# Kernel tuning notes

Hardware: AMD Instinct MI355X
Metric: run time of the kernel (lower is better)

Reference implementation:

```python
import jax, jax.numpy as jnp
import numpy as np

HEADS = 16
HIDDEN = 1024
DH = HIDDEN // HEADS
STD = 0.02


def setup_inputs() -> dict:
    key = jax.random.key(0)
    ks = jax.random.split(key, 12)
    B, S = 4, 2048
    inp = {
        'q': jax.random.normal(ks[0], (B, S, HIDDEN), jnp.float32),
        'k': jax.random.normal(ks[1], (B, S, HIDDEN), jnp.float32),
        'v': jax.random.normal(ks[2], (B, S, HIDDEN), jnp.float32),
        'mask': jax.random.randint(ks[3], (B, S), 0, 2, jnp.int32),
        # linear layers: weight [out,in] torch-style, init N(0, 0.02), bias 0
        'wq': STD * jax.random.normal(ks[4], (HIDDEN, HIDDEN), jnp.float32),
        'bq': jnp.zeros((HIDDEN,), jnp.float32),
        'wk': STD * jax.random.normal(ks[5], (HIDDEN, HIDDEN), jnp.float32),
        'bk': jnp.zeros((HIDDEN,), jnp.float32),
        'wv': STD * jax.random.normal(ks[6], (HIDDEN, HIDDEN), jnp.float32),
        'bv': jnp.zeros((HIDDEN,), jnp.float32),
        'wo': STD * jax.random.normal(ks[7], (HIDDEN, HIDDEN), jnp.float32),
        'bo': jnp.zeros((HIDDEN,), jnp.float32),
    }
    return inp


def _split_heads(x):
    B, S, _ = x.shape
    return x.reshape(B, S, HEADS, DH).transpose(0, 2, 1, 3)  # [B,H,S,dh]


def reference(q, k, v, mask, wq, bq, wk, bk, wv, bv, wo, bo):
    B, S, _ = q.shape
    qh = _split_heads(q @ wq.T + bq)
    kh = _split_heads(k @ wk.T + bk)
    vh = _split_heads(v @ wv.T + bv)
    scale = 1.0 / jnp.sqrt(jnp.float32(DH))
    corr = jnp.einsum('bhqd,bhkd->bhqk', qh, kh) * scale  # [B,H,S,S]
    # original masks QUERY rows: mask [B,S] -> [B,1,S,1] broadcast over heads & keys
    row_mask = (mask != 0)[:, None, :, None]
    corr = jnp.where(row_mask, corr, jnp.float32(-1e9))
    prob = jax.nn.softmax(corr, axis=-1)
    # dropout p=0.0 (eval / deterministic reference)
    hidden = jnp.einsum('bhqk,bhkd->bhqd', prob, vh)
    hidden = hidden.transpose(0, 2, 1, 3).reshape(B, S, HIDDEN)
    return hidden @ wo.T + bo
```

## Files before the change

kernel.cpp:

```cpp
#include <hip/hip_runtime.h>

#define BATCH 4
#define SEQ 2048
#define HEADS 16
#define DHEAD 64
#define HID 1024
#define MROWS (BATCH * SEQ)
#define QSCALE 0.1803368801111092f

typedef unsigned short u16;
typedef unsigned int u32;
typedef __attribute__((ext_vector_type(4))) float f32x4;
typedef __attribute__((ext_vector_type(8))) short bf16x8;

#define MFMA16(a, b, c) __builtin_amdgcn_mfma_f32_16x16x32_bf16((a), (b), (c), 0, 0, 0)
#define EXP2F(x) __builtin_amdgcn_exp2f(x)

__device__ __forceinline__ u16 f2bf(float f) {
  union { float f; u32 i; } x; x.f = f;
  u32 r = x.i + 0x7fffu + ((x.i >> 16) & 1u);
  return (u16)(r >> 16);
}

__device__ __forceinline__ void lds16(const u16* g, u16* s) {
  __builtin_amdgcn_global_load_lds(
      (const __attribute__((address_space(1))) void*)g,
      (__attribute__((address_space(3))) void*)s, 16, 0, 0);
}

__device__ __forceinline__ void stage8f(const float* __restrict__ g, u16* s) {
  const float4 a = *(const float4*)g;
  const float4 b = *(const float4*)(g + 4);
  ushort4 lo, hi;
  lo.x = f2bf(a.x); lo.y = f2bf(a.y); lo.z = f2bf(a.z); lo.w = f2bf(a.w);
  hi.x = f2bf(b.x); hi.y = f2bf(b.y); hi.z = f2bf(b.z); hi.w = f2bf(b.w);
  *(ushort4*)s = lo;
  *(ushort4*)(s + 4) = hi;
}

struct CvtArgs {
  const float* src[7];
  u16* dst[7];
};
__global__ __launch_bounds__(256) void cvt7(CvtArgs args, int yoff, int nact) {
  const int y = blockIdx.y + yoff;
  const int i = (blockIdx.x * 256 + threadIdx.x) * 8;
  if (y < 3) {
    if (i < nact) stage8f(args.src[y] + i, args.dst[y] + i);
  } else {
    if (i < 4 * (1 << 20)) {
      const int j = i >> 20, off = i & ((1 << 20) - 1);
      stage8f(args.src[3 + j] + off, args.dst[3 + j] + off);
    }
  }
}

template<bool ADMA, bool BDMA>
__device__ __forceinline__ void gemm_core(
    const void* __restrict__ Av, const void* __restrict__ Wv,
    int tid, int m0, int n0, u16* As, u16* Bs, f32x4 (&acc)[4][4])
{
  const int srow = tid >> 2, cslot = tid & 3;
  const int gc = cslot ^ ((srow >> 1) & 3);
  const int w = tid >> 6, l = tid & 63;
  const int quad = l >> 4, l15 = l & 15;
  const int sw = (l15 >> 1) & 3;
  const int wm = (w & 1) << 6, wn = (w >> 1) << 6;

  for (int k0 = 0; k0 < HID; k0 += 32) {
    if (ADMA) {
      const u16* ag = (const u16*)Av + (size_t)(m0 + srow) * HID + k0 + gc * 8;
      lds16(ag, &As[tid * 8]);
      lds16(ag + (size_t)64 * HID, &As[2048 + tid * 8]);
    } else {
      const float* ag = (const float*)Av + (size_t)(m0 + srow) * HID + k0 + gc * 8;
      stage8f(ag, &As[srow * 32 + cslot * 8]);
      stage8f(ag + (size_t)64 * HID, &As[(64 + srow) * 32 + cslot * 8]);
    }
    if (BDMA) {
      const u16* bg = (const u16*)Wv + (size_t)(n0 + srow) * HID + k0 + gc * 8;
      lds16(bg, &Bs[tid * 8]);
      lds16(bg + (size_t)64 * HID, &Bs[2048 + tid * 8]);
    } else {
      const float* bg = (const float*)Wv + (size_t)(n0 + srow) * HID + k0 + gc * 8;
      stage8f(bg, &Bs[srow * 32 + cslot * 8]);
      stage8f(bg + (size_t)64 * HID, &Bs[(64 + srow) * 32 + cslot * 8]);
    }
    __syncthreads();

    bf16x8 a[4], b[4];
    #pragma unroll
    for (int i = 0; i < 4; ++i)
      a[i] = *(const bf16x8*)&As[(wm + i * 16 + l15) * 32 + (quad ^ sw) * 8];
    #pragma unroll
    for (int j = 0; j < 4; ++j)
      b[j] = *(const bf16x8*)&Bs[(wn + j * 16 + l15) * 32 + (quad ^ sw) * 8];
    #pragma unroll
    for (int i = 0; i < 4; ++i)
      #pragma unroll
      for (int j = 0; j < 4; ++j)
        acc[i][j] = MFMA16(a[i], b[j], acc[i][j]);
    __syncthreads();
  }
}

template<bool ADMA, bool BDMA>
__global__ __launch_bounds__(256) void gemm_qkv(
    const void* __restrict__ xq, const void* __restrict__ xk,
    const void* __restrict__ xv,
    const void* __restrict__ wqv, const void* __restrict__ wkv,
    const void* __restrict__ wvv,
    const float* __restrict__ bq, const float* __restrict__ bk,
    const float* __restrict__ bv, const int* __restrict__ Mask,
    u16* __restrict__ qh, u16* __restrict__ kh, u16* __restrict__ vt)
{
  __shared__ u16 As[128 * 32];
  __shared__ u16 Bs[128 * 32];
  const int z = blockIdx.z;
  const void* A = (z == 0) ? xq : (z == 1) ? xk : xv;
  const void* W = (z == 0) ? wqv : (z == 1) ? wkv : wvv;
  const float* Bias = (z == 0) ? bq : (z == 1) ? bk : bv;

  const int tid = threadIdx.x;
  const int m0 = blockIdx.x << 7, n0 = blockIdx.y << 7;
  f32x4 acc[4][4] = {};
  gemm_core<ADMA, BDMA>(A, W, tid, m0, n0, As, Bs, acc);

  const int w = tid >> 6, l = tid & 63;
  const int quad = l >> 4, l15 = l & 15;
  const int wm = (w & 1) << 6, wn = (w >> 1) << 6;

  if (z <= 1) {
    u16* Out = (z == 0) ? qh : kh;
    #pragma unroll
    for (int i = 0; i < 4; ++i) {
      float fl[4];
      #pragma unroll
      for (int r = 0; r < 4; ++r) {
        const int m = m0 + wm + i * 16 + (quad << 2) + r;
        fl[r] = (z == 0) ? (Mask[m] ? QSCALE : 0.f) : 1.f;
      }
      #pragma unroll
      for (int j = 0; j < 4; ++j) {
        const int n = n0 + wn + j * 16 + l15;
        const float bias = Bias[n];
        const int h = n >> 6, d = n & 63;
        #pragma unroll
        for (int r = 0; r < 4; ++r) {
          const int m = m0 + wm + i * 16 + (quad << 2) + r;
          const int bb = m >> 11, s = m & (SEQ - 1);
          Out[((size_t)(bb * HEADS + h) * SEQ + s) * DHEAD + d] =
              f2bf((acc[i][j][r] + bias) * fl[r]);
        }
      }
    }
  } else {
    const int sblk = (m0 + wm) & (SEQ - 1);
    const int bb = (m0 + wm) >> 11;
    #pragma unroll
    for (int j = 0; j < 4; ++j) {
      const int n = n0 + wn + j * 16 + l15;
      const float bias = Bias[n];
      const int h = n >> 6, d = n & 63;
      u16* base = vt + ((size_t)(bb * HEADS + h) * DHEAD + d) * SEQ + sblk;
      #pragma unroll
      for (int r = 0; r < 4; ++r) {
        ushort4 pk;
        pk.x = f2bf(acc[0][j][r] + bias);
        pk.y = f2bf(acc[1][j][r] + bias);
        pk.z = f2bf(acc[2][j][r] + bias);
        pk.w = f2bf(acc[3][j][r] + bias);
        *(ushort4*)(base + ((quad << 2) + r) * 4) = pk;
      }
    }
  }
}

template<bool BDMA>
__global__ __launch_bounds__(256) void gemm_out(
    const u16* __restrict__ hidden, const void* __restrict__ wov,
    const float* __restrict__ bo, float* __restrict__ Out)
{
  __shared__ u16 As[128 * 32];
  __shared__ u16 Bs[128 * 32];
  const int tid = threadIdx.x;
  const int m0 = blockIdx.x << 7, n0 = blockIdx.y << 7;
  f32x4 acc[4][4] = {};
  gemm_core<true, BDMA>(hidden, wov, tid, m0, n0, As, Bs, acc);

  const int w = tid >> 6, l = tid & 63;
  const int quad = l >> 4, l15 = l & 15;
  const int wm = (w & 1) << 6, wn = (w >> 1) << 6;
  #pragma unroll
  for (int j = 0; j < 4; ++j) {
    const int n = n0 + wn + j * 16 + l15;
    const float bias = bo[n];
    #pragma unroll
    for (int i = 0; i < 4; ++i) {
      const int mb = m0 + wm + i * 16 + (quad << 2);
      #pragma unroll
      for (int r = 0; r < 4; ++r)
        Out[(size_t)(mb + r) * HID + n] = acc[i][j][r] + bias;
    }
  }
}

__global__ __launch_bounds__(128, 2) void attn_mfma(
    const u16* __restrict__ QH, const u16* __restrict__ KH,
    const u16* __restrict__ VT, u16* __restrict__ Hidden)
{
  __shared__ u16 QP[128 * 64];
  __shared__ u16 Ks[2][64 * 32];
  __shared__ u16 Vt[2][64 * 32];

  const int tid = threadIdx.x;
  const int w = tid >> 6, l = tid & 63;
  const int quad = l >> 4, l15 = l & 15;
  const int sw = (l15 >> 1) & 3;
  const int srow = tid >> 2, cslot = tid & 3;
  const int gc = cslot ^ ((srow >> 1) & 3);

  const int lin = blockIdx.y * 16 + blockIdx.x;
  const int bh = lin & 63, b = bh >> 4, h = bh & 15;
  const int q0 = (lin >> 6) << 7;

  const u16* qbase = QH + (size_t)bh * SEQ * DHEAD;
  const u16* kbase = KH + (size_t)bh * SEQ * DHEAD;
  const u16* vbase = VT + (size_t)bh * DHEAD * SEQ;

  #pragma unroll
  for (int hh = 0; hh < 2; ++hh)
    #pragma unroll
    for (int part = 0; part < 4; ++part)
      lds16(qbase + (size_t)(q0 + part * 32 + srow) * DHEAD + hh * 32 + gc * 8,
            &QP[hh * 4096 + part * 1024 + tid * 8]);
  __syncthreads();

  bf16x8 aq[2][4];
  #pragma unroll
  for (int hh = 0; hh < 2; ++hh)
    #pragma unroll
    for (int i = 0; i < 4; ++i)
      aq[hh][i] = *(const bf16x8*)
          &QP[hh * 4096 + (w * 64 + i * 16 + l15) * 32 + (quad ^ sw) * 8];

  float lsum[4][4] = {};
  f32x4 o[4][4] = {};

  for (int t0 = 0; t0 < SEQ; t0 += 64) {
    __syncthreads();
    #pragma unroll
    for (int hh = 0; hh < 2; ++hh)
      #pragma unroll
      for (int part = 0; part < 2; ++part) {
        lds16(kbase + (size_t)(t0 + part * 32 + srow) * DHEAD + hh * 32 + gc * 8,
              &Ks[hh][part * 1024 + tid * 8]);
        lds16(vbase + (size_t)(part * 32 + srow) * SEQ + t0 + hh * 32 + gc * 8,
              &Vt[hh][part * 1024 + tid * 8]);
      }
    __syncthreads();

    f32x4 s[4][4] = {};
    #pragma unroll
    for (int j = 0; j < 4; ++j)
      #pragma unroll
      for (int hh = 0; hh < 2; ++hh) {
        const bf16x8 bk = *(const bf16x8*)
            &Ks[hh][(j * 16 + l15) * 32 + (quad ^ sw) * 8];
        #pragma unroll
        for (int i = 0; i < 4; ++i)
          s[i][j] = MFMA16(aq[hh][i], bk, s[i][j]);
      }

    #pragma unroll
    for (int i = 0; i < 4; ++i)
      #pragma unroll
      for (int r = 0; r < 4; ++r) {
        const float p0 = EXP2F(s[i][0][r]);
        const float p1 = EXP2F(s[i][1][r]);
        const float p2 = EXP2F(s[i][2][r]);
        const float p3 = EXP2F(s[i][3][r]);
        lsum[i][r] += (p0 + p1) + (p2 + p3);
        const int row = w * 64 + i * 16 + (quad << 2) + r;
        const int cs = ((l15 >> 1) ^ (row & 7)) * 8 + (l15 & 1) * 4;
        ushort4 pk;
        pk.x = f2bf(p0); pk.y = f2bf(p1); pk.z = f2bf(p2); pk.w = f2bf(p3);
        *(ushort4*)&QP[row * 64 + cs] = pk;
      }

    #pragma unroll
    for (int hh = 0; hh < 2; ++hh) {
      bf16x8 ap[4];
      #pragma unroll
      for (int i = 0; i < 4; ++i) {
        const int row = w * 64 + i * 16 + l15;
        ap[i] = *(const bf16x8*)
            &QP[row * 64 + (((hh * 4 + quad) ^ (row & 7)) << 3)];
      }
      #pragma unroll
      for (int j = 0; j < 4; ++j) {
        const bf16x8 vb = *(const bf16x8*)
            &Vt[hh][(j * 16 + l15) * 32 + (quad ^ sw) * 8];
        #pragma unroll
        for (int i = 0; i < 4; ++i)
          o[i][j] = MFMA16(ap[i], vb, o[i][j]);
      }
    }
  }

  float inv[4][4];
  #pragma unroll
  for (int i = 0; i < 4; ++i)
    #pragma unroll
    for (int r = 0; r < 4; ++r) {
      float t = lsum[i][r];
      #pragma unroll
      for (int off = 1; off < 16; off <<= 1)
        t += __shfl_xor(t, off);
      inv[i][r] = 1.f / t;
    }

  #pragma unroll
  for (int i = 0; i < 4; ++i)
    #pragma unroll
    for (int j = 0; j < 4; ++j)
      #pragma unroll
      for (int r = 0; r < 4; ++r) {
        const int qrow = q0 + w * 64 + i * 16 + (quad << 2) + r;
        Hidden[((size_t)(b * SEQ + qrow)) * HID + h * DHEAD + j * 16 + l15] =
            f2bf(o[i][j][r] * inv[i][r]);
      }
}

extern "C" void kernel_launch(void* const* d_in, const int* in_sizes, int n_in,
                              void* d_out, int out_size, void* d_ws, size_t ws_size,
                              hipStream_t stream) {
  const float* q  = (const float*)d_in[0];
  const float* k  = (const float*)d_in[1];
  const float* v  = (const float*)d_in[2];
  const int* mask = (const int*)d_in[3];
  const float* wq = (const float*)d_in[4];
  const float* bq = (const float*)d_in[5];
  const float* wk = (const float*)d_in[6];
  const float* bk = (const float*)d_in[7];
  const float* wv = (const float*)d_in[8];
  const float* bv = (const float*)d_in[9];
  const float* wo = (const float*)d_in[10];
  const float* bo = (const float*)d_in[11];

  const size_t SEG = (size_t)MROWS * HID;
  const size_t WSEG = (size_t)HID * HID;
  const dim3 gq(MROWS / 128, HID / 128, 3);
  const dim3 go(MROWS / 128, HID / 128);
  const dim3 ga(SEQ / 128, BATCH * HEADS);

  const size_t planFULL = (6 * SEG + 4 * WSEG) * sizeof(u16);
  const size_t planMID  = (4 * SEG + 4 * WSEG) * sizeof(u16);

  if (ws_size >= planFULL) {
    u16* qb  = (u16*)d_ws;
    u16* kb  = qb + SEG;
    u16* vb  = kb + SEG;
    u16* qh  = vb + SEG;
    u16* kh  = qh + SEG;
    u16* vt  = kh + SEG;
    u16* wqb = vt + SEG;
    u16* wkb = wqb + WSEG;
    u16* wvb = wkb + WSEG;
    u16* wob = wvb + WSEG;
    u16* hidden = qb;

    CvtArgs ca;
    ca.src[0] = q;  ca.dst[0] = qb;
    ca.src[1] = k;  ca.dst[1] = kb;
    ca.src[2] = v;  ca.dst[2] = vb;
    ca.src[3] = wq; ca.dst[3] = wqb;
    ca.src[4] = wk; ca.dst[4] = wkb;
    ca.src[5] = wv; ca.dst[5] = wvb;
    ca.src[6] = wo; ca.dst[6] = wob;
    cvt7<<<dim3(SEG / 2048, 4), 256, 0, stream>>>(ca, 0, (int)SEG);

    gemm_qkv<true, true><<<gq, 256, 0, stream>>>(qb, kb, vb, wqb, wkb, wvb,
                                                 bq, bk, bv, mask, qh, kh, vt);
    attn_mfma<<<ga, 128, 0, stream>>>(qh, kh, vt, hidden);
    gemm_out<true><<<go, 256, 0, stream>>>(hidden, wob, bo, (float*)d_out);
  } else if (ws_size >= planMID) {
    u16* wqb = (u16*)d_ws;
    u16* wkb = wqb + WSEG;
    u16* wvb = wkb + WSEG;
    u16* wob = wvb + WSEG;
    u16* qh = wob + WSEG;
    u16* kh = qh + SEG;
    u16* vt = kh + SEG;
    u16* hidden = vt + SEG;

    CvtArgs ca;
    ca.src[0] = ca.src[1] = ca.src[2] = q;
    ca.dst[0] = ca.dst[1] = ca.dst[2] = wqb;
    ca.src[3] = wq; ca.dst[3] = wqb;
    ca.src[4] = wk; ca.dst[4] = wkb;
    ca.src[5] = wv; ca.dst[5] = wvb;
    ca.src[6] = wo; ca.dst[6] = wob;
    cvt7<<<dim3(4 * WSEG / 2048, 1), 256, 0, stream>>>(ca, 3, 0);

    gemm_qkv<false, true><<<gq, 256, 0, stream>>>(q, k, v, wqb, wkb, wvb,
                                                  bq, bk, bv, mask, qh, kh, vt);
    attn_mfma<<<ga, 128, 0, stream>>>(qh, kh, vt, hidden);
    gemm_out<true><<<go, 256, 0, stream>>>(hidden, wob, bo, (float*)d_out);
  } else {
    u16* qh = (u16*)d_ws;
    u16* kh = qh + SEG;
    u16* vt = kh + SEG;
    u16* hidden = vt + SEG;

    gemm_qkv<false, false><<<gq, 256, 0, stream>>>(q, k, v, wq, wk, wv,
                                                   bq, bk, bv, mask, qh, kh, vt);
    attn_mfma<<<ga, 128, 0, stream>>>(qh, kh, vt, hidden);
    gemm_out<false><<<go, 256, 0, stream>>>(hidden, wo, bo, (float*)d_out);
  }
}
```

Before: 358.0 us.

## Software-pipeline K/V loads in attention loop with double-buffered V and vmcnt waits

Restructures the attention main loop so the next K tile and the next V tile are issued with async global-to-LDS loads right after the QK^T MFMAs. V is double-buffered, and explicit s_waitcnt vmcnt counts with raw barriers replace the full __syncthreads pairs, so loads overlap the softmax and PV compute. It also adds s_setprio around the MFMA phases and replaces the manual bf16 rounding with the packed v_cvt_pk_bf16_f32 instruction in the V projection epilogue and the P store. This relies on careful vmcnt accounting: the last iteration issues a wraparound prefetch that is never used, which adds extra loads.

```diff
diff --git a/kernel.cpp b/kernel.cpp
--- a/kernel.cpp
+++ b/kernel.cpp
@@ -12,6 +12,7 @@
 typedef unsigned int u32;
 typedef __attribute__((ext_vector_type(4))) float f32x4;
 typedef __attribute__((ext_vector_type(8))) short bf16x8;
+typedef __attribute__((ext_vector_type(2))) unsigned int u32x2;
 
 #define MFMA16(a, b, c) __builtin_amdgcn_mfma_f32_16x16x32_bf16((a), (b), (c), 0, 0, 0)
 #define EXP2F(x) __builtin_amdgcn_exp2f(x)
@@ -20,6 +21,12 @@
   union { float f; u32 i; } x; x.f = f;
   u32 r = x.i + 0x7fffu + ((x.i >> 16) & 1u);
   return (u16)(r >> 16);
+}
+
+__device__ __forceinline__ u32 cvtpk(float a, float b) {
+  u32 d;
+  asm("v_cvt_pk_bf16_f32 %0, %1, %2" : "=v"(d) : "v"(a), "v"(b));
+  return d;
 }
 
 __device__ __forceinline__ void lds16(const u16* g, u16* s) {
@@ -165,12 +172,10 @@
       u16* base = vt + ((size_t)(bb * HEADS + h) * DHEAD + d) * SEQ + sblk;
       #pragma unroll
       for (int r = 0; r < 4; ++r) {
-        ushort4 pk;
-        pk.x = f2bf(acc[0][j][r] + bias);
-        pk.y = f2bf(acc[1][j][r] + bias);
-        pk.z = f2bf(acc[2][j][r] + bias);
-        pk.w = f2bf(acc[3][j][r] + bias);
-        *(ushort4*)(base + ((quad << 2) + r) * 4) = pk;
+        u32x2 pk;
+        pk.x = cvtpk(acc[0][j][r] + bias, acc[1][j][r] + bias);
+        pk.y = cvtpk(acc[2][j][r] + bias, acc[3][j][r] + bias);
+        *(u32x2*)(base + ((quad << 2) + r) * 4) = pk;
       }
     }
   }
@@ -210,8 +215,8 @@
     const u16* __restrict__ VT, u16* __restrict__ Hidden)
 {
   __shared__ u16 QP[128 * 64];
-  __shared__ u16 Ks[2][64 * 32];
-  __shared__ u16 Vt[2][64 * 32];
+  __shared__ u16 Ks[2][2048];
+  __shared__ u16 Vt[2][2][2048];
 
   const int tid = threadIdx.x;
   const int w = tid >> 6, l = tid & 63;
@@ -234,7 +239,20 @@
     for (int part = 0; part < 4; ++part)
       lds16(qbase + (size_t)(q0 + part * 32 + srow) * DHEAD + hh * 32 + gc * 8,
             &QP[hh * 4096 + part * 1024 + tid * 8]);
-  __syncthreads();
+  #pragma unroll
+  for (int hh = 0; hh < 2; ++hh)
+    #pragma unroll
+    for (int part = 0; part < 2; ++part)
+      lds16(kbase + (size_t)(part * 32 + srow) * DHEAD + hh * 32 + gc * 8,
+            &Ks[hh][part * 1024 + tid * 8]);
+  #pragma unroll
+  for (int hh = 0; hh < 2; ++hh)
+    #pragma unroll
+    for (int part = 0; part < 2; ++part)
+      lds16(vbase + (size_t)(part * 32 + srow) * SEQ + hh * 32 + gc * 8,
+            &Vt[0][hh][part * 1024 + tid * 8]);
+  asm volatile("s_waitcnt vmcnt(8)" ::: "memory");
+  __builtin_amdgcn_s_barrier();
 
   bf16x8 aq[2][4];
   #pragma unroll
@@ -246,21 +264,14 @@
 
   float lsum[4][4] = {};
   f32x4 o[4][4] = {};
-
-  for (int t0 = 0; t0 < SEQ; t0 += 64) {
-    __syncthreads();
-    #pragma unroll
-    for (int hh = 0; hh < 2; ++hh)
-      #pragma unroll
-      for (int part = 0; part < 2; ++part) {
-        lds16(kbase + (size_t)(t0 + part * 32 + srow) * DHEAD + hh * 32 + gc * 8,
-              &Ks[hh][part * 1024 + tid * 8]);
-        lds16(vbase + (size_t)(part * 32 + srow) * SEQ + t0 + hh * 32 + gc * 8,
-              &Vt[hh][part * 1024 + tid * 8]);
-      }
-    __syncthreads();
+  int cur = 0;
+
+  for (int it = 0; it < SEQ / 64; ++it) {
+    asm volatile("s_waitcnt vmcnt(4)" ::: "memory");
+    __builtin_amdgcn_s_barrier();
 
     f32x4 s[4][4] = {};
+    __builtin_amdgcn_s_setprio(1);
     #pragma unroll
     for (int j = 0; j < 4; ++j)
       #pragma unroll
@@ -271,6 +282,22 @@
         for (int i = 0; i < 4; ++i)
           s[i][j] = MFMA16(aq[hh][i], bk, s[i][j]);
       }
+    __builtin_amdgcn_s_setprio(0);
+    __builtin_amdgcn_s_barrier();
+
+    const int tn = ((it + 1) & (SEQ / 64 - 1)) << 6;
+    #pragma unroll
+    for (int hh = 0; hh < 2; ++hh)
+      #pragma unroll
+      for (int part = 0; part < 2; ++part)
+        lds16(kbase + (size_t)(tn + part * 32 + srow) * DHEAD + hh * 32 + gc * 8,
+              &Ks[hh][part * 1024 + tid * 8]);
+    #pragma unroll
+    for (int hh = 0; hh < 2; ++hh)
+      #pragma unroll
+      for (int part = 0; part < 2; ++part)
+        lds16(vbase + (size_t)(part * 32 + srow) * SEQ + tn + hh * 32 + gc * 8,
+              &Vt[cur ^ 1][hh][part * 1024 + tid * 8]);
 
     #pragma unroll
     for (int i = 0; i < 4; ++i)
@@ -283,11 +310,16 @@
         lsum[i][r] += (p0 + p1) + (p2 + p3);
         const int row = w * 64 + i * 16 + (quad << 2) + r;
         const int cs = ((l15 >> 1) ^ (row & 7)) * 8 + (l15 & 1) * 4;
-        ushort4 pk;
-        pk.x = f2bf(p0); pk.y = f2bf(p1); pk.z = f2bf(p2); pk.w = f2bf(p3);
-        *(ushort4*)&QP[row * 64 + cs] = pk;
-      }
-
+        u32x2 pk;
+        pk.x = cvtpk(p0, p1);
+        pk.y = cvtpk(p2, p3);
+        *(u32x2*)&QP[row * 64 + cs] = pk;
+      }
+
+    asm volatile("s_waitcnt vmcnt(8)" ::: "memory");
+    __builtin_amdgcn_s_barrier();
+
+    __builtin_amdgcn_s_setprio(1);
     #pragma unroll
     for (int hh = 0; hh < 2; ++hh) {
       bf16x8 ap[4];
@@ -300,13 +332,16 @@
       #pragma unroll
       for (int j = 0; j < 4; ++j) {
         const bf16x8 vb = *(const bf16x8*)
-            &Vt[hh][(j * 16 + l15) * 32 + (quad ^ sw) * 8];
+            &Vt[cur][hh][(j * 16 + l15) * 32 + (quad ^ sw) * 8];
         #pragma unroll
         for (int i = 0; i < 4; ++i)
           o[i][j] = MFMA16(ap[i], vb, o[i][j]);
       }
     }
-  }
+    __builtin_amdgcn_s_setprio(0);
+    cur ^= 1;
+  }
+  asm volatile("s_waitcnt vmcnt(0)" ::: "memory");
 
   float inv[4][4];
   #pragma unroll
```

Measured after the change: 343.0 us. 1.04x faster.
